# Performance work log

Measured on AMD Instinct MI355X. Metric: run time of the kernel, lower is better.

## Reference

```python
import jax, jax.numpy as jnp
import numpy as np

B, S, E, D = 4, 2048, 1024, 512


def setup_inputs() -> dict:
    key = jax.random.key(0)
    ks = jax.random.split(key, 7)
    s_in = 1.0 / np.sqrt(E)
    return {
        "x": jax.random.normal(ks[0], (B, S, E), dtype=jnp.float32),
        "wq": jax.random.uniform(ks[1], (E, D), jnp.float32, -s_in, s_in),
        "bq": jax.random.uniform(ks[2], (D,), jnp.float32, -s_in, s_in),
        "wk": jax.random.uniform(ks[3], (E, D), jnp.float32, -s_in, s_in),
        "bk": jax.random.uniform(ks[4], (D,), jnp.float32, -s_in, s_in),
        "wv": jax.random.uniform(ks[5], (E, D), jnp.float32, -s_in, s_in),
        "bv": jax.random.uniform(ks[6], (D,), jnp.float32, -s_in, s_in),
    }


def reference(x, wq, bq, wk, bk, wv, bv):
    # QKV projections: [B,S,E] @ [E,D] -> [B,S,D]
    q = jnp.einsum('bse,ed->bsd', x, wq) + bq
    k = jnp.einsum('bse,ed->bsd', x, wk) + bk
    v = jnp.einsum('bse,ed->bsd', x, wv) + bv
    # scores [B,S,S]
    scores = jnp.einsum('bqd,bkd->bqk', q, k)
    # causal mask applied before scaling (as in original; -inf unaffected by scale)
    causal = jnp.tril(jnp.ones((S, S), dtype=bool))
    scores = jnp.where(causal[None], scores, -jnp.inf)
    scores = scores / jnp.sqrt(jnp.float32(D))
    attn = jax.nn.softmax(scores, axis=-1)
    return jnp.einsum('bqk,bkd->bqd', attn, v)
```

## Files before the change

kernel.cpp:

```cpp
#include <hip/hip_runtime.h>
#include <math.h>


typedef __attribute__((ext_vector_type(4))) float f32x4;
typedef __attribute__((ext_vector_type(16))) float f32x16;
typedef __attribute__((ext_vector_type(8))) short bf16x8;
typedef __attribute__((ext_vector_type(8))) unsigned short u16x8;

#define B_ 4
#define S_ 2048
#define E_ 1024
#define D_ 512

__device__ __forceinline__ unsigned short f2bf(float f) {
  unsigned u = __float_as_uint(f);
  u += 0x7fffu + ((u >> 16) & 1u);
  return (unsigned short)(u >> 16);
}

__device__ __forceinline__ float bf2f(unsigned short h) {
  return __uint_as_float(((unsigned)h) << 16);
}

template<int N> __device__ __forceinline__ void wait_vm() {
  if constexpr (N == 0)      asm volatile("s_waitcnt vmcnt(0)" ::: "memory");
  else if constexpr (N == 3) asm volatile("s_waitcnt vmcnt(3)" ::: "memory");
  else if constexpr (N == 4) asm volatile("s_waitcnt vmcnt(4)" ::: "memory");
  else if constexpr (N == 5) asm volatile("s_waitcnt vmcnt(5)" ::: "memory");
  else if constexpr (N == 6) asm volatile("s_waitcnt vmcnt(6)" ::: "memory");
  else static_assert(N != N, "unsupported vmcnt");
}


template<int ROWS, int NTHR>
__device__ __forceinline__ void stage_tile32(const unsigned short* __restrict__ g, long ld,
                                             long rowBase, int kBase,
                                             unsigned short* lds, int tid) {
  constexpr int CALLS = (ROWS * 64) / (NTHR * 16);
  #pragma unroll
  for (int i = 0; i < CALLS; ++i) {
    int idx = i * NTHR + tid;
    int row = idx >> 2, cc = idx & 3;
    int src_g = cc ^ ((row >> 1) & 3);
    __builtin_amdgcn_global_load_lds(
      (const __attribute__((address_space(1))) void*)(g + (rowBase + row) * ld + kBase + src_g * 8),
      (__attribute__((address_space(3))) void*)(lds + idx * 8),
      16, 0, 0);
  }
}

template<int MT, int NTT>
__device__ __forceinline__ void compute_tile32(const unsigned short* As, const unsigned short* Bs,
                                               int a_row0, int b_row0, int lane,
                                               f32x16 (&acc)[MT][NTT]) {
  int lr = lane & 31, lhalf = lane >> 5;
  int p = (lr >> 1) & 3;
  #pragma unroll
  for (int ki = 0; ki < 2; ++ki) {
    int slot = ((ki * 2 + lhalf) ^ p) * 8;
    bf16x8 af[MT], bf[NTT];
    #pragma unroll
    for (int mt = 0; mt < MT; ++mt)
      af[mt] = *(const bf16x8*)(As + (a_row0 + mt * 32 + lr) * 32 + slot);
    #pragma unroll
    for (int nt = 0; nt < NTT; ++nt)
      bf[nt] = *(const bf16x8*)(Bs + (b_row0 + nt * 32 + lr) * 32 + slot);
    #pragma unroll
    for (int mt = 0; mt < MT; ++mt)
      #pragma unroll
      for (int nt = 0; nt < NTT; ++nt)
        acc[mt][nt] = __builtin_amdgcn_mfma_f32_32x32x16_bf16(af[mt], bf[nt], acc[mt][nt], 0, 0, 0);
  }
}

template<int AROWS, int BROWS, int NTHR, int MT, int NTT>
__device__ __forceinline__ void mainloop32(
    const unsigned short* __restrict__ A, long lda, long rowA,
    const unsigned short* __restrict__ Bt, long ldb, long rowB,
    int nsteps, unsigned short* AsBuf, unsigned short* BsBuf,
    int tid, int lane, int a_row0, int b_row0, f32x16 (&acc)[MT][NTT]) {
  constexpr int ASZ = AROWS * 32, BSZ = BROWS * 32;
  constexpr int LPS = (AROWS * 64) / (NTHR * 16) + (BROWS * 64) / (NTHR * 16);
  unsigned short *a0 = AsBuf, *a1 = AsBuf + ASZ, *a2 = AsBuf + 2 * ASZ;
  unsigned short *b0 = BsBuf, *b1 = BsBuf + BSZ, *b2 = BsBuf + 2 * BSZ;
  stage_tile32<AROWS, NTHR>(A, lda, rowA, 0, a0, tid);
  stage_tile32<BROWS, NTHR>(Bt, ldb, rowB, 0, b0, tid);
  if (nsteps > 1) {
    stage_tile32<AROWS, NTHR>(A, lda, rowA, 32, a1, tid);
    stage_tile32<BROWS, NTHR>(Bt, ldb, rowB, 32, b1, tid);
  }
  for (int t = 0; t < nsteps; ++t) {
    if (t < nsteps - 1) wait_vm<LPS>(); else wait_vm<0>();
    __builtin_amdgcn_s_barrier();
    __builtin_amdgcn_sched_barrier(0);
    compute_tile32<MT, NTT>(a0, b0, a_row0, b_row0, lane, acc);
    if (t + 2 < nsteps) {
      stage_tile32<AROWS, NTHR>(A, lda, rowA, (t + 2) * 32, a2, tid);
      stage_tile32<BROWS, NTHR>(Bt, ldb, rowB, (t + 2) * 32, b2, tid);
    }
    unsigned short* ta = a0; a0 = a1; a1 = a2; a2 = ta;
    unsigned short* tb = b0; b0 = b1; b1 = b2; b2 = tb;
  }
}

__device__ __forceinline__ void compute_pv64(const unsigned short* As, const unsigned short* Bs,
                                             int a_row0, int b_row0, int lane, bf16x8 ones,
                                             f32x16 (&acc)[2], f32x16& accl) {
  int lr = lane & 31, lhalf = lane >> 5;
  int p = (lr >> 1) & 3;
  #pragma unroll
  for (int ki = 0; ki < 2; ++ki) {
    int slot = ((ki * 2 + lhalf) ^ p) * 8;
    bf16x8 af  = *(const bf16x8*)(As + (a_row0 + lr) * 32 + slot);
    bf16x8 bf0 = *(const bf16x8*)(Bs + (b_row0 + lr) * 32 + slot);
    bf16x8 bf1 = *(const bf16x8*)(Bs + (b_row0 + 32 + lr) * 32 + slot);
    accl   = __builtin_amdgcn_mfma_f32_32x32x16_bf16(af, ones, accl, 0, 0, 0);
    acc[0] = __builtin_amdgcn_mfma_f32_32x32x16_bf16(af, bf0, acc[0], 0, 0, 0);
    acc[1] = __builtin_amdgcn_mfma_f32_32x32x16_bf16(af, bf1, acc[1], 0, 0, 0);
  }
}

__device__ __forceinline__ void pv_mainloop64(
    const unsigned short* __restrict__ A, long rowA,
    const unsigned short* __restrict__ Bt, long rowB,
    int nsteps, unsigned short (*As)[64 * 32], unsigned short (*Bs)[128 * 32],
    int tid, int lane, int a_row0, int b_row0,
    f32x16 (&acc)[2], f32x16& accl) {
  bf16x8 ones;
  #pragma unroll
  for (int j = 0; j < 8; ++j) ones[j] = (short)0x3F80;
  stage_tile32<64, 256>(A, S_, rowA, 0, As[0], tid);
  stage_tile32<128, 256>(Bt, S_, rowB, 0, Bs[0], tid);
  if (nsteps > 1) {
    stage_tile32<64, 256>(A, S_, rowA, 32, As[1], tid);
    stage_tile32<128, 256>(Bt, S_, rowB, 32, Bs[1], tid);
  }
  if (nsteps > 2) {
    stage_tile32<64, 256>(A, S_, rowA, 64, As[2], tid);
    stage_tile32<128, 256>(Bt, S_, rowB, 64, Bs[2], tid);
  }
  for (int t = 0; t < nsteps; ++t) {
    int rem = nsteps - t;
    if (rem > 2)      wait_vm<6>();
    else if (rem == 2) wait_vm<3>();
    else               wait_vm<0>();
    __builtin_amdgcn_s_barrier();
    __builtin_amdgcn_sched_barrier(0);
    compute_pv64(As[t & 3], Bs[t & 3], a_row0, b_row0, lane, ones, acc, accl);
    if (t + 3 < nsteps) {
      stage_tile32<64, 256>(A, S_, rowA, (t + 3) * 32, As[(t + 3) & 3], tid);
      stage_tile32<128, 256>(Bt, S_, rowB, (t + 3) * 32, Bs[(t + 3) & 3], tid);
    }
  }
}


__global__ __launch_bounds__(256) void convert_f32_bf16(const float* __restrict__ src,
                                                        unsigned short* __restrict__ dst) {
  long i = (long)blockIdx.x * 256 + threadIdx.x;
  f32x4 a = ((const f32x4*)src)[2 * i];
  f32x4 b = ((const f32x4*)src)[2 * i + 1];
  u16x8 o;
  #pragma unroll
  for (int j = 0; j < 4; ++j) { o[j] = f2bf(a[j]); o[4 + j] = f2bf(b[j]); }
  ((u16x8*)dst)[i] = o;
}

__global__ __launch_bounds__(256) void build_wT(const float* __restrict__ wq,
                                                const float* __restrict__ wk,
                                                const float* __restrict__ wv,
                                                unsigned short* __restrict__ wbT) {
  int o = blockIdx.x * 256 + threadIdx.x;
  int n = o >> 10, k = o & 1023;
  const float* w = (n < 512) ? wq : ((n < 1024) ? wk : wv);
  int d = n & 511;
  wbT[o] = f2bf(w[(long)k * 512 + d]);
}

__global__ __launch_bounds__(256, 3) void qkv_gemm(
    const unsigned short* __restrict__ xb, const unsigned short* __restrict__ wbT,
    const float* __restrict__ bq, const float* __restrict__ bk, const float* __restrict__ bv,
    unsigned short* __restrict__ qb, unsigned short* __restrict__ kb,
    unsigned short* __restrict__ vb) {
  __shared__ unsigned short As[3][128 * 32], Bs[3][128 * 32];
  int tid = threadIdx.x, wave = tid >> 6, lane = tid & 63;
  int wm = wave >> 1, wn = wave & 1;
  int wg = blockIdx.x;
  int swz = (wg & 7) * 96 + (wg >> 3);
  int nb = swz % 12, mb = swz / 12;
  long rowA = (long)mb * 128, rowB = (long)nb * 128;
  f32x16 acc[2][2] = {};
  mainloop32<128, 128, 256, 2, 2>(xb, E_, rowA, wbT, E_, rowB, E_ / 32,
                                  &As[0][0], &Bs[0][0], tid, lane, wm * 64, wn * 64, acc);
  int lc = lane & 31, lhi = (lane >> 5) * 4;
  #pragma unroll
  for (int nt = 0; nt < 2; ++nt) {
    int n = (int)rowB + wn * 64 + nt * 32 + lc;
    int d = n & 511;
    float bias; unsigned short* dst;
    if (n < 512)       { bias = bq[d]; dst = qb; }
    else if (n < 1024) { bias = bk[d]; dst = kb; }
    else               { bias = bv[d]; dst = vb; }
    #pragma unroll
    for (int mt = 0; mt < 2; ++mt) {
      long mbase = rowA + wm * 64 + mt * 32 + lhi;
      #pragma unroll
      for (int r = 0; r < 16; ++r) {
        long m = mbase + (r & 3) + 8 * (r >> 2);
        dst[m * D_ + d] = f2bf(acc[mt][nt][r] + bias);
      }
    }
  }
}

__global__ __launch_bounds__(256) void transpose_v(const unsigned short* __restrict__ vb,
                                                   unsigned short* __restrict__ vtb) {
  int dblk = blockIdx.x;
  int sblk = blockIdx.y;
  int b = blockIdx.z;
  __shared__ unsigned short ls[64][72];
  int tid = threadIdx.x;
  int r = tid >> 3, c8 = (tid & 7) * 8;
  long d0 = (long)dblk * 64, s0 = (long)sblk * 64;
  #pragma unroll
  for (int p = 0; p < 2; ++p) {
    u16x8 v = *(const u16x8*)(vb + ((long)b * S_ + s0 + r + p * 32) * D_ + d0 + c8);
    *(u16x8*)&ls[r + p * 32][c8] = v;
  }
  __syncthreads();
  #pragma unroll
  for (int p = 0; p < 2; ++p) {
    int d = r + p * 32;
    u16x8 o;
    #pragma unroll
    for (int j = 0; j < 8; ++j) o[j] = ls[c8 + j][d];
    *(u16x8*)(vtb + ((long)b * D_ + d0 + d) * S_ + s0 + c8) = o;
  }
}

__global__ __launch_bounds__(256, 4) void scores_gemm(
    const unsigned short* __restrict__ qb, const unsigned short* __restrict__ kb,
    unsigned short* __restrict__ sc) {
  int jb = blockIdx.x, im = 31 - blockIdx.y, b = blockIdx.z;
  if (2 * jb > im) return;
  __shared__ unsigned short As[3][64 * 32], Bs[3][128 * 32];
  int tid = threadIdx.x, wave = tid >> 6, lane = tid & 63;
  int wm = wave >> 1, wn = wave & 1;
  const unsigned short* A  = qb + (long)b * S_ * D_;
  const unsigned short* Bt = kb + (long)b * S_ * D_;
  long rowA = (long)im * 64, rowB = (long)jb * 128;
  f32x16 acc[1][2] = {};
  mainloop32<64, 128, 256, 1, 2>(A, D_, rowA, Bt, D_, rowB, D_ / 32,
                                 &As[0][0], &Bs[0][0], tid, lane, wm * 32, wn * 64, acc);
  unsigned short* po = sc + (long)b * S_ * S_;
  const float cexp = 1.4426950408889634f / 22.627416997969522f;
  int lc = lane & 31, lhi = (lane >> 5) * 4;
  long mbase = rowA + wm * 32 + lhi;
  #pragma unroll
  for (int r = 0; r < 16; ++r) {
    long m = mbase + (r & 3) + 8 * (r >> 2);
    #pragma unroll
    for (int nt = 0; nt < 2; ++nt) {
      long n = rowB + wn * 64 + nt * 32 + lc;
      float p = (n <= m) ? exp2f(acc[0][nt][r] * cexp) : 0.f;
      po[m * S_ + n] = f2bf(p);
    }
  }
}

__global__ __launch_bounds__(256, 3) void pv_gemm(
    const unsigned short* __restrict__ sc, const unsigned short* __restrict__ vtb,
    float* __restrict__ out) {
  int bn = blockIdx.x, bm = 31 - blockIdx.y, b = blockIdx.z;
  __shared__ unsigned short As[4][64 * 32], Bs[4][128 * 32];
  int tid = threadIdx.x, wave = tid >> 6, lane = tid & 63;
  int wm = wave >> 1, wn = wave & 1;
  const unsigned short* A  = sc  + (long)b * S_ * S_;
  const unsigned short* Bt = vtb + (long)b * D_ * S_;
  long rowA = (long)bm * 64, rowB = (long)bn * 128;
  int nsteps = 2 * (bm + 1);
  f32x16 acc[2] = {};
  f32x16 accl = {};
  pv_mainloop64(A, rowA, Bt, rowB, nsteps, As, Bs, tid, lane,
                wm * 32, wn * 64, acc, accl);
  float* oo = out + (long)b * S_ * D_;
  int lc = lane & 31, lhi = (lane >> 5) * 4;
  long mbase = rowA + wm * 32 + lhi;
  #pragma unroll
  for (int r = 0; r < 16; ++r) {
    long m = mbase + (r & 3) + 8 * (r >> 2);
    float inv = 1.f / accl[r];
    #pragma unroll
    for (int nt = 0; nt < 2; ++nt) {
      long n = rowB + wn * 64 + nt * 32 + lc;
      oo[m * D_ + n] = acc[nt][r] * inv;
    }
  }
}

extern "C" void kernel_launch(void* const* d_in, const int* in_sizes, int n_in,
                              void* d_out, int out_size, void* d_ws, size_t ws_size,
                              hipStream_t stream) {
  const float* x   = (const float*)d_in[0];
  const float* wq  = (const float*)d_in[1];
  const float* bq  = (const float*)d_in[2];
  const float* wk  = (const float*)d_in[3];
  const float* bk  = (const float*)d_in[4];
  const float* wv  = (const float*)d_in[5];
  const float* bv  = (const float*)d_in[6];
  float* out = (float*)d_out;

  char* ws = (char*)d_ws;
  unsigned short* xb  = (unsigned short*)(ws);
  unsigned short* wbT = (unsigned short*)(ws + 16777216);
  unsigned short* qb  = (unsigned short*)(ws + 19922944);
  unsigned short* kb  = (unsigned short*)(ws + 28311552);
  unsigned short* vb  = (unsigned short*)(ws + 36700160);
  unsigned short* vtb = (unsigned short*)(ws + 45088768);
  unsigned short* sc  = (unsigned short*)(ws + 53477376);

  convert_f32_bf16<<<dim3(4096), dim3(256), 0, stream>>>(x, xb);
  build_wT<<<dim3(6144), dim3(256), 0, stream>>>(wq, wk, wv, wbT);
  qkv_gemm<<<dim3(768), dim3(256), 0, stream>>>(xb, wbT, bq, bk, bv, qb, kb, vb);
  transpose_v<<<dim3(8, 32, 4), dim3(256), 0, stream>>>(vb, vtb);
  scores_gemm<<<dim3(16, 32, 4), dim3(256), 0, stream>>>(qb, kb, sc);
  pv_gemm<<<dim3(4, 32, 4), dim3(256), 0, stream>>>(sc, vtb, out);
}
```

Before: 122.3 us.

## Widen PV GEMM K-tile to 64 with triple-buffered LDS pipeline

The PV GEMM now stages 64-wide K tiles using a new 8-chunk XOR swizzle. It keeps three LDS buffers in place of four 32-wide ones, which halves the number of barrier/wait iterations and doubles the MFMA work per synchronization. The LDS footprint per block grows (about 72 KB), so launch bounds drop from 3 to 2 blocks per CU, trading occupancy for fewer barriers. Pipeline depth falls from three tiles in flight to two.

```diff
diff --git a/kernel.cpp b/kernel.cpp
--- a/kernel.cpp
+++ b/kernel.cpp
@@ -26,7 +26,6 @@
   if constexpr (N == 0)      asm volatile("s_waitcnt vmcnt(0)" ::: "memory");
   else if constexpr (N == 3) asm volatile("s_waitcnt vmcnt(3)" ::: "memory");
   else if constexpr (N == 4) asm volatile("s_waitcnt vmcnt(4)" ::: "memory");
-  else if constexpr (N == 5) asm volatile("s_waitcnt vmcnt(5)" ::: "memory");
   else if constexpr (N == 6) asm volatile("s_waitcnt vmcnt(6)" ::: "memory");
   else static_assert(N != N, "unsupported vmcnt");
 }
@@ -103,17 +102,35 @@
   }
 }
 
+
+template<int ROWS, int NTHR>
+__device__ __forceinline__ void stage_tile64(const unsigned short* __restrict__ g, long ld,
+                                             long rowBase, int kBase,
+                                             unsigned short* lds, int tid) {
+  constexpr int CALLS = (ROWS * 128) / (NTHR * 16);
+  #pragma unroll
+  for (int i = 0; i < CALLS; ++i) {
+    int idx = i * NTHR + tid;
+    int row = idx >> 3, cc = idx & 7;
+    int src_g = cc ^ (row & 7);
+    __builtin_amdgcn_global_load_lds(
+      (const __attribute__((address_space(1))) void*)(g + (rowBase + row) * ld + kBase + src_g * 8),
+      (__attribute__((address_space(3))) void*)(lds + idx * 8),
+      16, 0, 0);
+  }
+}
+
 __device__ __forceinline__ void compute_pv64(const unsigned short* As, const unsigned short* Bs,
                                              int a_row0, int b_row0, int lane, bf16x8 ones,
                                              f32x16 (&acc)[2], f32x16& accl) {
   int lr = lane & 31, lhalf = lane >> 5;
-  int p = (lr >> 1) & 3;
-  #pragma unroll
-  for (int ki = 0; ki < 2; ++ki) {
+  int p = lr & 7;
+  #pragma unroll
+  for (int ki = 0; ki < 4; ++ki) {
     int slot = ((ki * 2 + lhalf) ^ p) * 8;
-    bf16x8 af  = *(const bf16x8*)(As + (a_row0 + lr) * 32 + slot);
-    bf16x8 bf0 = *(const bf16x8*)(Bs + (b_row0 + lr) * 32 + slot);
-    bf16x8 bf1 = *(const bf16x8*)(Bs + (b_row0 + 32 + lr) * 32 + slot);
+    bf16x8 af  = *(const bf16x8*)(As + (a_row0 + lr) * 64 + slot);
+    bf16x8 bf0 = *(const bf16x8*)(Bs + (b_row0 + lr) * 64 + slot);
+    bf16x8 bf1 = *(const bf16x8*)(Bs + (b_row0 + 32 + lr) * 64 + slot);
     accl   = __builtin_amdgcn_mfma_f32_32x32x16_bf16(af, ones, accl, 0, 0, 0);
     acc[0] = __builtin_amdgcn_mfma_f32_32x32x16_bf16(af, bf0, acc[0], 0, 0, 0);
     acc[1] = __builtin_amdgcn_mfma_f32_32x32x16_bf16(af, bf1, acc[1], 0, 0, 0);
@@ -123,34 +140,30 @@
 __device__ __forceinline__ void pv_mainloop64(
     const unsigned short* __restrict__ A, long rowA,
     const unsigned short* __restrict__ Bt, long rowB,
-    int nsteps, unsigned short (*As)[64 * 32], unsigned short (*Bs)[128 * 32],
+    int nsteps, unsigned short (*As)[64 * 64], unsigned short (*Bs)[128 * 64],
     int tid, int lane, int a_row0, int b_row0,
     f32x16 (&acc)[2], f32x16& accl) {
   bf16x8 ones;
   #pragma unroll
   for (int j = 0; j < 8; ++j) ones[j] = (short)0x3F80;
-  stage_tile32<64, 256>(A, S_, rowA, 0, As[0], tid);
-  stage_tile32<128, 256>(Bt, S_, rowB, 0, Bs[0], tid);
+  stage_tile64<64, 256>(A, S_, rowA, 0, As[0], tid);
+  stage_tile64<128, 256>(Bt, S_, rowB, 0, Bs[0], tid);
   if (nsteps > 1) {
-    stage_tile32<64, 256>(A, S_, rowA, 32, As[1], tid);
-    stage_tile32<128, 256>(Bt, S_, rowB, 32, Bs[1], tid);
-  }
-  if (nsteps > 2) {
-    stage_tile32<64, 256>(A, S_, rowA, 64, As[2], tid);
-    stage_tile32<128, 256>(Bt, S_, rowB, 64, Bs[2], tid);
-  }
+    stage_tile64<64, 256>(A, S_, rowA, 64, As[1], tid);
+    stage_tile64<128, 256>(Bt, S_, rowB, 64, Bs[1], tid);
+  }
+  int cur = 0;
   for (int t = 0; t < nsteps; ++t) {
-    int rem = nsteps - t;
-    if (rem > 2)      wait_vm<6>();
-    else if (rem == 2) wait_vm<3>();
-    else               wait_vm<0>();
+    if (t < nsteps - 1) wait_vm<6>(); else wait_vm<0>();
     __builtin_amdgcn_s_barrier();
     __builtin_amdgcn_sched_barrier(0);
-    compute_pv64(As[t & 3], Bs[t & 3], a_row0, b_row0, lane, ones, acc, accl);
-    if (t + 3 < nsteps) {
-      stage_tile32<64, 256>(A, S_, rowA, (t + 3) * 32, As[(t + 3) & 3], tid);
-      stage_tile32<128, 256>(Bt, S_, rowB, (t + 3) * 32, Bs[(t + 3) & 3], tid);
-    }
+    compute_pv64(As[cur], Bs[cur], a_row0, b_row0, lane, ones, acc, accl);
+    if (t + 2 < nsteps) {
+      int nxt = (cur + 2) % 3;
+      stage_tile64<64, 256>(A, S_, rowA, (t + 2) * 64, As[nxt], tid);
+      stage_tile64<128, 256>(Bt, S_, rowB, (t + 2) * 64, Bs[nxt], tid);
+    }
+    cur = (cur + 1) % 3;
   }
 }
 
@@ -268,17 +281,17 @@
   }
 }
 
-__global__ __launch_bounds__(256, 3) void pv_gemm(
+__global__ __launch_bounds__(256, 2) void pv_gemm(
     const unsigned short* __restrict__ sc, const unsigned short* __restrict__ vtb,
     float* __restrict__ out) {
   int bn = blockIdx.x, bm = 31 - blockIdx.y, b = blockIdx.z;
-  __shared__ unsigned short As[4][64 * 32], Bs[4][128 * 32];
+  __shared__ unsigned short As[3][64 * 64], Bs[3][128 * 64];
   int tid = threadIdx.x, wave = tid >> 6, lane = tid & 63;
   int wm = wave >> 1, wn = wave & 1;
   const unsigned short* A  = sc  + (long)b * S_ * S_;
   const unsigned short* Bt = vtb + (long)b * D_ * S_;
   long rowA = (long)bm * 64, rowB = (long)bn * 128;
-  int nsteps = 2 * (bm + 1);
+  int nsteps = bm + 1;
   f32x16 acc[2] = {};
   f32x16 accl = {};
   pv_mainloop64(A, rowA, Bt, rowB, nsteps, As, Bs, tid, lane,
```

Result: faster. 115.9 us (-5.3%).
